# Performance work log

Measured on AMD Instinct MI355X. Metric: run time of the kernel, lower is better.

Reference implementation:

```python
import jax, jax.numpy as jnp
import numpy as np

VOCAB = 100000
DIM = 128
BATCH = 65536
NEG = 5


def setup_inputs() -> dict:
    key = jax.random.key(0)
    k1, k2, k3, k4, k5 = jax.random.split(key, 5)
    # embedding tables initialized uniform(-1, 1) as in the torch module
    W_in = jax.random.uniform(k1, (VOCAB, DIM), dtype=jnp.float32, minval=-1.0, maxval=1.0)
    W_ctx = jax.random.uniform(k2, (VOCAB, DIM), dtype=jnp.float32, minval=-1.0, maxval=1.0)
    input_word = jax.random.randint(k3, (BATCH,), 0, VOCAB, dtype=jnp.int64)
    context_word = jax.random.randint(k4, (BATCH,), 0, VOCAB, dtype=jnp.int64)
    # multinomial over uniform noise_dist == uniform randint
    neg_idx = jax.random.randint(k5, (BATCH, NEG), 0, VOCAB, dtype=jnp.int64)
    return {
        "W_in": W_in,
        "W_ctx": W_ctx,
        "input_word": input_word,
        "context_word": context_word,
        "neg_idx": neg_idx,
    }


def reference(W_in, W_ctx, input_word, context_word, neg_idx):
    emb_input = W_in[input_word]            # [B, D]
    emb_context = W_ctx[context_word]       # [B, D]
    pos_score = jnp.sum(emb_input * emb_context, axis=1)       # [B]
    out_loss = jax.nn.log_sigmoid(pos_score)                   # [B]
    # NOTE: original torch code overwrites the context lookup with the
    # input-embedding lookup for negatives; we reproduce that faithfully.
    emb_negative = W_in[neg_idx]             # [B, K, D]
    neg_score = jnp.einsum('bkd,bd->bk', -emb_negative, emb_input)  # [B, K]
    noise_loss = jnp.sum(jax.nn.log_sigmoid(neg_score), axis=1)     # [B]
    total_loss = -jnp.mean(out_loss + noise_loss)
    return total_loss
```

## Files before the change

### kernel.cpp

```cpp
#include <hip/hip_runtime.h>

#define VOCAB 100000
#define DIM 128
#define BATCH 65536
#define NEG 5

#define BLOCKS 1024
#define TPB 256
#define GRPS_PER_BLK (TPB / 16)

__device__ __forceinline__ float log_sigmoid(float x) {
    return fminf(x, 0.0f) - log1pf(expf(-fabsf(x)));
}

__device__ __forceinline__ float dot4(float4 a, float4 b) {
    return a.x * b.x + a.y * b.y + a.z * b.z + a.w * b.w;
}

__global__ __launch_bounds__(TPB) void g2v_partial(
    const float* __restrict__ W_in, const float* __restrict__ W_ctx,
    const int* __restrict__ input_word, const int* __restrict__ context_word,
    const int* __restrict__ neg_idx, float* __restrict__ block_sums)
{
    const int lane16 = threadIdx.x & 15;
    const int grp_in_blk = threadIdx.x >> 4;
    const int grp = blockIdx.x * GRPS_PER_BLK + grp_in_blk;
    const int ngrp = gridDim.x * GRPS_PER_BLK;

    const float4* __restrict__ W_in4 = (const float4*)W_in;
    const float4* __restrict__ W_ctx4 = (const float4*)W_ctx;

    float gsum = 0.0f;

    for (int b = grp; b < BATCH; b += ngrp) {
        const int iw = input_word[b];
        const int cw = context_word[b];

        const float4* ri = W_in4 + iw * 32 + lane16;
        const float4 ei0 = ri[0];
        const float4 ei1 = ri[16];

        const float4* rc = W_ctx4 + cw * 32 + lane16;
        const float4 ec0 = rc[0];
        const float4 ec1 = rc[16];

        float pos = dot4(ei0, ec0) + dot4(ei1, ec1);

        float nd[NEG];
        #pragma unroll
        for (int k = 0; k < NEG; ++k) {
            const int nw = neg_idx[b * NEG + k];
            const float4* rn = W_in4 + nw * 32 + lane16;
            const float4 en0 = rn[0];
            const float4 en1 = rn[16];
            nd[k] = dot4(en0, ei0) + dot4(en1, ei1);
        }

        #pragma unroll
        for (int m = 1; m <= 8; m <<= 1) {
            pos += __shfl_xor(pos, m);
            #pragma unroll
            for (int k = 0; k < NEG; ++k) nd[k] += __shfl_xor(nd[k], m);
        }

        if (lane16 == 0) {
            float loss = log_sigmoid(pos);
            #pragma unroll
            for (int k = 0; k < NEG; ++k) loss += log_sigmoid(-nd[k]);
            gsum += loss;
        }
    }

    __shared__ float s[GRPS_PER_BLK];
    if (lane16 == 0) s[grp_in_blk] = gsum;
    __syncthreads();
    if (threadIdx.x == 0) {
        float t = 0.0f;
        #pragma unroll
        for (int i = 0; i < GRPS_PER_BLK; ++i) t += s[i];
        block_sums[blockIdx.x] = t;
    }
}

__global__ __launch_bounds__(256) void g2v_final(
    const float* __restrict__ block_sums, int n, float* __restrict__ out)
{
    __shared__ float s[256];
    float t = 0.0f;
    for (int i = threadIdx.x; i < n; i += 256) t += block_sums[i];
    s[threadIdx.x] = t;
    __syncthreads();
    for (int w = 128; w > 0; w >>= 1) {
        if (threadIdx.x < w) s[threadIdx.x] += s[threadIdx.x + w];
        __syncthreads();
    }
    if (threadIdx.x == 0) out[0] = -s[0] / (float)BATCH;
}

extern "C" void kernel_launch(void* const* d_in, const int* in_sizes, int n_in,
                              void* d_out, int out_size, void* d_ws, size_t ws_size,
                              hipStream_t stream) {
    const float* W_in        = (const float*)d_in[0];
    const float* W_ctx       = (const float*)d_in[1];
    const int*   input_word  = (const int*)d_in[2];
    const int*   context_word= (const int*)d_in[3];
    const int*   neg_idx     = (const int*)d_in[4];

    float* block_sums = (float*)d_ws;
    float* out        = (float*)d_out;

    g2v_partial<<<BLOCKS, TPB, 0, stream>>>(W_in, W_ctx, input_word,
                                            context_word, neg_idx, block_sums);
    g2v_final<<<1, 256, 0, stream>>>(block_sums, BLOCKS, out);
}
```

Measured before the change: 45.01 us.

## Bucket lookups by row index to localize gathers, stage input embeddings as bf16

Replaces the single fused gather kernel with a five-kernel pipeline. Lookups are scattered by atomics into buckets keyed by row index so that gathers from W_in and W_ctx touch nearby rows together. Input embeddings are gathered once and stored per batch item as bf16 in workspace, then reused by the positive and negative dot products. This adds kernel launches, atomics, extra workspace traffic and bf16 rounding error in the dot products. Lookups beyond the fixed overflow capacity are silently dropped.

```diff
diff --git a/kernel.cpp b/kernel.cpp
--- a/kernel.cpp
+++ b/kernel.cpp
@@ -5,92 +5,195 @@
 #define BATCH 65536
 #define NEG 5
 
-#define BLOCKS 1024
-#define TPB 256
-#define GRPS_PER_BLK (TPB / 16)
+#define NBKT 3125
+#define CAPA 32
+#define CAPC 32
+#define CAPN 128
+#define OVF  4096
+
+#define NGA  (NBKT*CAPA + OVF)
+#define NGC  (NBKT*CAPC)
+#define NGN  (NBKT*CAPN)
+#define NGBC (NGC + NGN + OVF + OVF)
+#define NPART (NGBC/16)
+
+#define NCUR (3*NBKT + 3)
 
 __device__ __forceinline__ float log_sigmoid(float x) {
     return fminf(x, 0.0f) - log1pf(expf(-fabsf(x)));
 }
-
 __device__ __forceinline__ float dot4(float4 a, float4 b) {
     return a.x * b.x + a.y * b.y + a.z * b.z + a.w * b.w;
 }
-
-__global__ __launch_bounds__(TPB) void g2v_partial(
+__device__ __forceinline__ unsigned bf16rne(float f) {
+    unsigned u = __float_as_uint(f);
+    return (u + 0x7fffu + ((u >> 16) & 1u)) >> 16;
+}
+__device__ __forceinline__ unsigned pack2(float a, float b) {
+    return bf16rne(a) | (bf16rne(b) << 16);
+}
+__device__ __forceinline__ float lo16(unsigned u) { return __uint_as_float(u << 16); }
+__device__ __forceinline__ float hi16(unsigned u) { return __uint_as_float(u & 0xffff0000u); }
+
+__device__ __forceinline__ int xcd_swz(int bid, int nblk) {
+    int q = nblk >> 3, r = nblk & 7;
+    int xcd = bid & 7, idx = bid >> 3;
+    return (xcd < r ? xcd * (q + 1) : r * (q + 1) + (xcd - r) * q) + idx;
+}
+
+#define E_OFF     0
+#define BKTA_OFF  16777216
+#define BKTC_OFF  17577216
+#define BKTN_OFF  18377216
+#define OVFA_OFF  21577216
+#define OVFC_OFF  21609984
+#define OVFN_OFF  21642752
+#define CUR_OFF   21675520
+#define PART_OFF  21713152
+
+__global__ __launch_bounds__(256) void k_zero(int* __restrict__ cur) {
+    int i = blockIdx.x * 256 + threadIdx.x;
+    if (i < NCUR) cur[i] = 0;
+}
+
+__global__ __launch_bounds__(256) void k_scatter(
+    const int* __restrict__ iw, const int* __restrict__ cw,
+    const int* __restrict__ negf,
+    uint2* __restrict__ bktA, uint2* __restrict__ bktC, uint2* __restrict__ bktN,
+    uint2* __restrict__ ovfA, uint2* __restrict__ ovfC, uint2* __restrict__ ovfN,
+    int* __restrict__ cur)
+{
+    int i = blockIdx.x * 256 + threadIdx.x;
+    int key, b, which;
+    if (i < BATCH)            { which = 0; b = i;             key = iw[b]; }
+    else if (i < 2 * BATCH)   { which = 1; b = i - BATCH;     key = cw[b]; }
+    else { int j = i - 2 * BATCH; which = 2; b = j / NEG;     key = negf[j]; }
+
+    int bkt = key >> 5;
+    uint2 ref = make_uint2((unsigned)key, (unsigned)b);
+    if (which == 0) {
+        int p = atomicAdd(&cur[bkt], 1);
+        if (p < CAPA) bktA[bkt * CAPA + p] = ref;
+        else { int q = atomicAdd(&cur[3 * NBKT + 0], 1); if (q < OVF) ovfA[q] = ref; }
+    } else if (which == 1) {
+        int p = atomicAdd(&cur[NBKT + bkt], 1);
+        if (p < CAPC) bktC[bkt * CAPC + p] = ref;
+        else { int q = atomicAdd(&cur[3 * NBKT + 1], 1); if (q < OVF) ovfC[q] = ref; }
+    } else {
+        int p = atomicAdd(&cur[2 * NBKT + bkt], 1);
+        if (p < CAPN) bktN[bkt * CAPN + p] = ref;
+        else { int q = atomicAdd(&cur[3 * NBKT + 2], 1); if (q < OVF) ovfN[q] = ref; }
+    }
+}
+
+__global__ __launch_bounds__(256) void k_phaseA(
+    const float* __restrict__ W_in, const uint2* __restrict__ bktA,
+    const uint2* __restrict__ ovfA, const int* __restrict__ cur,
+    ushort* __restrict__ E)
+{
+    const int lane16 = threadIdx.x & 15;
+    const int grp = threadIdx.x >> 4;
+    const int lbid = xcd_swz(blockIdx.x, NGA / 16);
+    const int g = lbid * 16 + grp;
+
+    bool valid = false;
+    uint2 ref;
+    if (g < NBKT * CAPA) {
+        int bkt = g >> 5, slot = g & 31;
+        int cnt = min(cur[bkt], CAPA);
+        if (slot < cnt) { valid = true; ref = bktA[g]; }
+    } else {
+        int j = g - NBKT * CAPA;
+        if (j < min(cur[3 * NBKT + 0], OVF)) { valid = true; ref = ovfA[j]; }
+    }
+    if (!valid) return;
+
+    const float4* __restrict__ W4 = (const float4*)W_in;
+    const int r = (int)ref.x;
+    const float4 f0 = W4[r * 32 + lane16];
+    const float4 f1 = W4[r * 32 + 16 + lane16];
+
+    uint4 v;
+    v.x = pack2(f0.x, f0.y);
+    v.y = pack2(f0.z, f0.w);
+    v.z = pack2(f1.x, f1.y);
+    v.w = pack2(f1.z, f1.w);
+    *(uint4*)(((char*)E) + (size_t)ref.y * 256 + lane16 * 16) = v;
+}
+
+__global__ __launch_bounds__(256) void k_phaseBC(
     const float* __restrict__ W_in, const float* __restrict__ W_ctx,
-    const int* __restrict__ input_word, const int* __restrict__ context_word,
-    const int* __restrict__ neg_idx, float* __restrict__ block_sums)
+    const uint2* __restrict__ bktC, const uint2* __restrict__ bktN,
+    const uint2* __restrict__ ovfC, const uint2* __restrict__ ovfN,
+    const int* __restrict__ cur, const ushort* __restrict__ E,
+    float* __restrict__ partials)
 {
     const int lane16 = threadIdx.x & 15;
-    const int grp_in_blk = threadIdx.x >> 4;
-    const int grp = blockIdx.x * GRPS_PER_BLK + grp_in_blk;
-    const int ngrp = gridDim.x * GRPS_PER_BLK;
-
-    const float4* __restrict__ W_in4 = (const float4*)W_in;
-    const float4* __restrict__ W_ctx4 = (const float4*)W_ctx;
-
-    float gsum = 0.0f;
-
-    for (int b = grp; b < BATCH; b += ngrp) {
-        const int iw = input_word[b];
-        const int cw = context_word[b];
-
-        const float4* ri = W_in4 + iw * 32 + lane16;
-        const float4 ei0 = ri[0];
-        const float4 ei1 = ri[16];
-
-        const float4* rc = W_ctx4 + cw * 32 + lane16;
-        const float4 ec0 = rc[0];
-        const float4 ec1 = rc[16];
-
-        float pos = dot4(ei0, ec0) + dot4(ei1, ec1);
-
-        float nd[NEG];
+    const int grp = threadIdx.x >> 4;
+    const int lbid = xcd_swz(blockIdx.x, NGBC / 16);
+    const int g = lbid * 16 + grp;
+
+    bool valid = false;
+    float sign = 1.0f;
+    const float* tbl = W_ctx;
+    uint2 ref;
+    if (g < NGC) {
+        int bkt = g >> 5, slot = g & 31;
+        int cnt = min(cur[NBKT + bkt], CAPC);
+        if (slot < cnt) { valid = true; ref = bktC[g]; }
+    } else if (g < NGC + NGN) {
+        int q = g - NGC;
+        int bkt = q >> 7, slot = q & 127;
+        int cnt = min(cur[2 * NBKT + bkt], CAPN);
+        if (slot < cnt) { valid = true; ref = bktN[q]; }
+        tbl = W_in; sign = -1.0f;
+    } else if (g < NGC + NGN + OVF) {
+        int j = g - (NGC + NGN);
+        if (j < min(cur[3 * NBKT + 1], OVF)) { valid = true; ref = ovfC[j]; }
+    } else {
+        int j = g - (NGC + NGN + OVF);
+        if (j < min(cur[3 * NBKT + 2], OVF)) { valid = true; ref = ovfN[j]; }
+        tbl = W_in; sign = -1.0f;
+    }
+
+    float loss = 0.0f;
+    if (valid) {
+        const float4* __restrict__ T4 = (const float4*)tbl;
+        const int r = (int)ref.x;
+        const float4 t0 = T4[r * 32 + lane16];
+        const float4 t1 = T4[r * 32 + 16 + lane16];
+        const uint4 ev = *(const uint4*)(((const char*)E) + (size_t)ref.y * 256 + lane16 * 16);
+
+        float4 e0 = make_float4(lo16(ev.x), hi16(ev.x), lo16(ev.y), hi16(ev.y));
+        float4 e1 = make_float4(lo16(ev.z), hi16(ev.z), lo16(ev.w), hi16(ev.w));
+        float d = dot4(t0, e0) + dot4(t1, e1);
+
         #pragma unroll
-        for (int k = 0; k < NEG; ++k) {
-            const int nw = neg_idx[b * NEG + k];
-            const float4* rn = W_in4 + nw * 32 + lane16;
-            const float4 en0 = rn[0];
-            const float4 en1 = rn[16];
-            nd[k] = dot4(en0, ei0) + dot4(en1, ei1);
-        }
-
-        #pragma unroll
-        for (int m = 1; m <= 8; m <<= 1) {
-            pos += __shfl_xor(pos, m);
-            #pragma unroll
-            for (int k = 0; k < NEG; ++k) nd[k] += __shfl_xor(nd[k], m);
-        }
-
-        if (lane16 == 0) {
-            float loss = log_sigmoid(pos);
-            #pragma unroll
-            for (int k = 0; k < NEG; ++k) loss += log_sigmoid(-nd[k]);
-            gsum += loss;
-        }
-    }
-
-    __shared__ float s[GRPS_PER_BLK];
-    if (lane16 == 0) s[grp_in_blk] = gsum;
+        for (int m = 1; m <= 8; m <<= 1) d += __shfl_xor(d, m);
+
+        if (lane16 == 0) loss = log_sigmoid(sign * d);
+    }
+
+    __shared__ float s[16];
+    if (lane16 == 0) s[grp] = loss;
     __syncthreads();
     if (threadIdx.x == 0) {
         float t = 0.0f;
         #pragma unroll
-        for (int i = 0; i < GRPS_PER_BLK; ++i) t += s[i];
-        block_sums[blockIdx.x] = t;
-    }
-}
-
-__global__ __launch_bounds__(256) void g2v_final(
-    const float* __restrict__ block_sums, int n, float* __restrict__ out)
-{
-    __shared__ float s[256];
+        for (int i = 0; i < 16; ++i) t += s[i];
+        partials[lbid] = t;
+    }
+}
+
+__global__ __launch_bounds__(1024) void k_final(
+    const float* __restrict__ partials, float* __restrict__ out)
+{
+    __shared__ float s[1024];
     float t = 0.0f;
-    for (int i = threadIdx.x; i < n; i += 256) t += block_sums[i];
+    for (int i = threadIdx.x; i < NPART; i += 1024) t += partials[i];
     s[threadIdx.x] = t;
     __syncthreads();
-    for (int w = 128; w > 0; w >>= 1) {
+    for (int w = 512; w > 0; w >>= 1) {
         if (threadIdx.x < w) s[threadIdx.x] += s[threadIdx.x + w];
         __syncthreads();
     }
@@ -100,16 +203,29 @@
 extern "C" void kernel_launch(void* const* d_in, const int* in_sizes, int n_in,
                               void* d_out, int out_size, void* d_ws, size_t ws_size,
                               hipStream_t stream) {
-    const float* W_in        = (const float*)d_in[0];
-    const float* W_ctx       = (const float*)d_in[1];
-    const int*   input_word  = (const int*)d_in[2];
-    const int*   context_word= (const int*)d_in[3];
-    const int*   neg_idx     = (const int*)d_in[4];
-
-    float* block_sums = (float*)d_ws;
-    float* out        = (float*)d_out;
-
-    g2v_partial<<<BLOCKS, TPB, 0, stream>>>(W_in, W_ctx, input_word,
-                                            context_word, neg_idx, block_sums);
-    g2v_final<<<1, 256, 0, stream>>>(block_sums, BLOCKS, out);
-}
+    const float* W_in   = (const float*)d_in[0];
+    const float* W_ctx  = (const float*)d_in[1];
+    const int*   iw     = (const int*)d_in[2];
+    const int*   cw     = (const int*)d_in[3];
+    const int*   negf   = (const int*)d_in[4];
+
+    char* w = (char*)d_ws;
+    ushort* E      = (ushort*)(w + E_OFF);
+    uint2*  bktA   = (uint2*)(w + BKTA_OFF);
+    uint2*  bktC   = (uint2*)(w + BKTC_OFF);
+    uint2*  bktN   = (uint2*)(w + BKTN_OFF);
+    uint2*  ovfA   = (uint2*)(w + OVFA_OFF);
+    uint2*  ovfC   = (uint2*)(w + OVFC_OFF);
+    uint2*  ovfN   = (uint2*)(w + OVFN_OFF);
+    int*    cur    = (int*)(w + CUR_OFF);
+    float*  parts  = (float*)(w + PART_OFF);
+    float*  out    = (float*)d_out;
+
+    k_zero<<<(NCUR + 255) / 256, 256, 0, stream>>>(cur);
+    k_scatter<<<(7 * BATCH) / 256, 256, 0, stream>>>(iw, cw, negf,
+                bktA, bktC, bktN, ovfA, ovfC, ovfN, cur);
+    k_phaseA<<<NGA / 16, 256, 0, stream>>>(W_in, bktA, ovfA, cur, E);
+    k_phaseBC<<<NGBC / 16, 256, 0, stream>>>(W_in, W_ctx, bktC, bktN,
+                ovfC, ovfN, cur, E, parts);
+    k_final<<<1, 1024, 0, stream>>>(parts, out);
+}
```

After: 103.8 us. 131% more time.

## Pipeline embedding gathers through LDS with async global_load_lds double buffering

Applied to the files above, without the earlier changes.

Each wave prefetches all indices for its 8 samples up front, then issues direct global-to-LDS 16-byte loads for two samples per slot into a double-buffered LDS region, computing one slot while the next loads with explicit vmcnt waits. Rows are split across 32-lane halves so each lane handles one float4 per row. Grid size doubles and the final reduction uses 1024 threads. This aims to raise memory-level parallelism of the random row gathers at the cost of LDS use and hand-scheduled waits.

```diff
diff --git a/kernel.cpp b/kernel.cpp
--- a/kernel.cpp
+++ b/kernel.cpp
@@ -5,92 +5,143 @@
 #define BATCH 65536
 #define NEG 5
 
-#define BLOCKS 1024
 #define TPB 256
-#define GRPS_PER_BLK (TPB / 16)
+#define WAVES 4
+#define BLOCKS 2048
+#define ITERS 4
+#define SLOT_BYTES 7168
+#define ROWB 512
+
+typedef __attribute__((address_space(1))) void gvoid;
+typedef __attribute__((address_space(3))) void lvoid;
 
 __device__ __forceinline__ float log_sigmoid(float x) {
     return fminf(x, 0.0f) - log1pf(expf(-fabsf(x)));
 }
-
 __device__ __forceinline__ float dot4(float4 a, float4 b) {
     return a.x * b.x + a.y * b.y + a.z * b.z + a.w * b.w;
 }
+__device__ __forceinline__ void gload_lds16(const void* g, void* l) {
+    __builtin_amdgcn_global_load_lds((gvoid*)g, (lvoid*)l, 16, 0, 0);
+}
+
+#define ISSUE_SLOT(it)                                                         \
+    {                                                                          \
+        char* dst = mybuf + ((it) & 1) * SLOT_BYTES;                           \
+        _Pragma("unroll")                                                      \
+        for (int j = 0; j < 7; ++j) {                                          \
+            const int r = half ? rows[it][2 * j + 1] : rows[it][2 * j];        \
+            const float* tb =                                                  \
+                ((j == 0 && half) || (j == 4 && !half)) ? W_ctx : W_in;        \
+            const char* src = (const char*)(tb + (size_t)r * DIM) + l32 * 16;  \
+            gload_lds16(src, dst + j * 1024);                                  \
+        }                                                                      \
+    }
+
+#define COMPUTE_SLOT(it)                                                       \
+    {                                                                          \
+        const char* base =                                                     \
+            mybuf + ((it) & 1) * SLOT_BYTES + half * 3584 + l32 * 16;          \
+        const float4 ei = *(const float4*)(base + 0 * ROWB);                   \
+        const float4 ec = *(const float4*)(base + 1 * ROWB);                   \
+        float pos_s = dot4(ei, ec);                                            \
+        float nd[NEG];                                                         \
+        _Pragma("unroll")                                                      \
+        for (int k = 0; k < NEG; ++k) {                                        \
+            const float4 en = *(const float4*)(base + (2 + k) * ROWB);         \
+            nd[k] = dot4(en, ei);                                              \
+        }                                                                      \
+        _Pragma("unroll")                                                      \
+        for (int m = 1; m <= 16; m <<= 1) {                                    \
+            pos_s += __shfl_xor(pos_s, m);                                     \
+            _Pragma("unroll")                                                  \
+            for (int k = 0; k < NEG; ++k) nd[k] += __shfl_xor(nd[k], m);       \
+        }                                                                      \
+        if (l32 == 0) {                                                        \
+            float loss = log_sigmoid(pos_s);                                   \
+            _Pragma("unroll")                                                  \
+            for (int k = 0; k < NEG; ++k) loss += log_sigmoid(-nd[k]);         \
+            acc += loss;                                                       \
+        }                                                                      \
+    }
+
+#define WAITV(n)                                                               \
+    asm volatile("s_waitcnt vmcnt(" #n ")" ::: "memory");                      \
+    __builtin_amdgcn_sched_barrier(0);
+
+#define FENCE() __builtin_amdgcn_sched_barrier(0);
 
 __global__ __launch_bounds__(TPB) void g2v_partial(
     const float* __restrict__ W_in, const float* __restrict__ W_ctx,
     const int* __restrict__ input_word, const int* __restrict__ context_word,
     const int* __restrict__ neg_idx, float* __restrict__ block_sums)
 {
-    const int lane16 = threadIdx.x & 15;
-    const int grp_in_blk = threadIdx.x >> 4;
-    const int grp = blockIdx.x * GRPS_PER_BLK + grp_in_blk;
-    const int ngrp = gridDim.x * GRPS_PER_BLK;
+    __shared__ __align__(16) char ldsraw[WAVES * 2 * SLOT_BYTES];
+    __shared__ float swave[WAVES];
 
-    const float4* __restrict__ W_in4 = (const float4*)W_in;
-    const float4* __restrict__ W_ctx4 = (const float4*)W_ctx;
+    const int tid = threadIdx.x;
+    const int wid = tid >> 6;
+    const int lane = tid & 63;
+    const int half = lane >> 5;
+    const int l32 = lane & 31;
+    const int gw = blockIdx.x * WAVES + wid;
 
-    float gsum = 0.0f;
+    char* mybuf = ldsraw + wid * (2 * SLOT_BYTES);
 
-    for (int b = grp; b < BATCH; b += ngrp) {
-        const int iw = input_word[b];
-        const int cw = context_word[b];
+    int rows[ITERS][14];
+    #pragma unroll
+    for (int it = 0; it < ITERS; ++it) {
+        const int b0 = (gw * ITERS + it) * 2;
+        rows[it][0] = input_word[b0];
+        rows[it][1] = context_word[b0];
+        #pragma unroll
+        for (int k = 0; k < NEG; ++k) rows[it][2 + k] = neg_idx[b0 * NEG + k];
+        rows[it][7] = input_word[b0 + 1];
+        rows[it][8] = context_word[b0 + 1];
+        #pragma unroll
+        for (int k = 0; k < NEG; ++k) rows[it][9 + k] = neg_idx[(b0 + 1) * NEG + k];
+    }
+    asm volatile("s_waitcnt vmcnt(0)" ::: "memory");
+    __builtin_amdgcn_sched_barrier(0);
 
-        const float4* ri = W_in4 + iw * 32 + lane16;
-        const float4 ei0 = ri[0];
-        const float4 ei1 = ri[16];
+    float acc = 0.0f;
 
-        const float4* rc = W_ctx4 + cw * 32 + lane16;
-        const float4 ec0 = rc[0];
-        const float4 ec1 = rc[16];
+    ISSUE_SLOT(0)
+    ISSUE_SLOT(1)
 
-        float pos = dot4(ei0, ec0) + dot4(ei1, ec1);
+    WAITV(7)
+    COMPUTE_SLOT(0)
+    FENCE()
+    ISSUE_SLOT(2)
 
-        float nd[NEG];
-        #pragma unroll
-        for (int k = 0; k < NEG; ++k) {
-            const int nw = neg_idx[b * NEG + k];
-            const float4* rn = W_in4 + nw * 32 + lane16;
-            const float4 en0 = rn[0];
-            const float4 en1 = rn[16];
-            nd[k] = dot4(en0, ei0) + dot4(en1, ei1);
-        }
+    WAITV(7)
+    COMPUTE_SLOT(1)
+    FENCE()
+    ISSUE_SLOT(3)
 
-        #pragma unroll
-        for (int m = 1; m <= 8; m <<= 1) {
-            pos += __shfl_xor(pos, m);
-            #pragma unroll
-            for (int k = 0; k < NEG; ++k) nd[k] += __shfl_xor(nd[k], m);
-        }
+    WAITV(7)
+    COMPUTE_SLOT(2)
 
-        if (lane16 == 0) {
-            float loss = log_sigmoid(pos);
-            #pragma unroll
-            for (int k = 0; k < NEG; ++k) loss += log_sigmoid(-nd[k]);
-            gsum += loss;
-        }
-    }
+    WAITV(0)
+    COMPUTE_SLOT(3)
 
-    __shared__ float s[GRPS_PER_BLK];
-    if (lane16 == 0) s[grp_in_blk] = gsum;
+    acc += __shfl_xor(acc, 32);
+    if (lane == 0) swave[wid] = acc;
     __syncthreads();
-    if (threadIdx.x == 0) {
-        float t = 0.0f;
-        #pragma unroll
-        for (int i = 0; i < GRPS_PER_BLK; ++i) t += s[i];
-        block_sums[blockIdx.x] = t;
+    if (tid == 0) {
+        block_sums[blockIdx.x] = swave[0] + swave[1] + swave[2] + swave[3];
     }
 }
 
-__global__ __launch_bounds__(256) void g2v_final(
+__global__ __launch_bounds__(1024) void g2v_final(
     const float* __restrict__ block_sums, int n, float* __restrict__ out)
 {
-    __shared__ float s[256];
+    __shared__ float s[1024];
     float t = 0.0f;
-    for (int i = threadIdx.x; i < n; i += 256) t += block_sums[i];
+    for (int i = threadIdx.x; i < n; i += 1024) t += block_sums[i];
     s[threadIdx.x] = t;
     __syncthreads();
-    for (int w = 128; w > 0; w >>= 1) {
+    for (int w = 512; w > 0; w >>= 1) {
         if (threadIdx.x < w) s[threadIdx.x] += s[threadIdx.x + w];
         __syncthreads();
     }
@@ -100,16 +151,16 @@
 extern "C" void kernel_launch(void* const* d_in, const int* in_sizes, int n_in,
                               void* d_out, int out_size, void* d_ws, size_t ws_size,
                               hipStream_t stream) {
-    const float* W_in        = (const float*)d_in[0];
-    const float* W_ctx       = (const float*)d_in[1];
-    const int*   input_word  = (const int*)d_in[2];
-    const int*   context_word= (const int*)d_in[3];
-    const int*   neg_idx     = (const int*)d_in[4];
+    const float* W_in         = (const float*)d_in[0];
+    const float* W_ctx        = (const float*)d_in[1];
+    const int*   input_word   = (const int*)d_in[2];
+    const int*   context_word = (const int*)d_in[3];
+    const int*   neg_idx      = (const int*)d_in[4];
 
     float* block_sums = (float*)d_ws;
     float* out        = (float*)d_out;
 
     g2v_partial<<<BLOCKS, TPB, 0, stream>>>(W_in, W_ctx, input_word,
                                             context_word, neg_idx, block_sums);
-    g2v_final<<<1, 256, 0, stream>>>(block_sums, BLOCKS, out);
+    g2v_final<<<1, 1024, 0, stream>>>(block_sums, BLOCKS, out);
 }
```

Result: slower. 67.77 us (+50.6%).
